# Performance work log

Hardware: AMD Instinct MI355X
Metric: run time of the kernel (lower is better)

The kernel has to match this reference:

```python
import jax, jax.numpy as jnp
import numpy as np

B, T, C, H = 4, 2048, 1024, 1024

def setup_inputs() -> dict:
    key = jax.random.key(0)
    ks = jax.random.split(key, 7)
    s = 0.02
    return {
        "x": jax.random.normal(ks[0], (B, T, C), dtype=jnp.float32),
        "k": jax.random.normal(ks[1], (B, T, C), dtype=jnp.float32),
        "q": jax.random.normal(ks[2], (B, T, C), dtype=jnp.float32),
        "v": jax.random.normal(ks[3], (B, T, C), dtype=jnp.float32),
        "Wk": jax.random.normal(ks[4], (C, H), dtype=jnp.float32) * s,
        "Wq": jax.random.normal(ks[5], (C, H), dtype=jnp.float32) * s,
        "Wv": jax.random.normal(ks[6], (C, H), dtype=jnp.float32) * s,
    }

def reference(x, k, q, v, Wk, Wq, Wv):
    Tcur = x.shape[1]
    kp = jnp.einsum('btc,ch->bth', k, Wk)
    qp = jnp.einsum('btc,ch->bth', q, Wq)
    # NOTE: original torch code (faithfully) projects v with the QUERY weights
    vp = jnp.einsum('btc,ch->bth', v, Wq)
    scale = jnp.asarray(H, jnp.float32) ** -0.5
    weights = jnp.einsum('bth,bsh->bts', qp, kp) * scale  # [B,T,T]
    causal = jnp.tril(jnp.ones((Tcur, Tcur), dtype=bool))
    weights = jnp.where(causal, weights, -jnp.inf)
    weights = jax.nn.softmax(weights, axis=-1)
    # dropout p=0.0 -> identity
    out = jnp.einsum('bts,bsh->bth', weights, vp)
    return out
```

## Files before the change

### kernel.cpp

```cpp
#include <hip/hip_runtime.h>
#include <stdint.h>
#include <math.h>

typedef unsigned short u16;
typedef __attribute__((ext_vector_type(8))) short short8;
typedef __attribute__((ext_vector_type(8))) u16 ushort8;
typedef __attribute__((ext_vector_type(4))) u16 u16x4;
typedef __attribute__((ext_vector_type(4))) float floatx4;

__device__ __forceinline__ u16 f2bf(float f) {
  union { float f; unsigned u; } c; c.f = f;
  unsigned u = c.u;
  return (u16)((u + 0x7fffu + ((u >> 16) & 1u)) >> 16);
}
__device__ __forceinline__ float bf2f(u16 h) {
  union { unsigned u; float f; } c; c.u = (unsigned)h << 16;
  return c.f;
}

__device__ __forceinline__ void async16(const u16* g, u16* l) {
  auto* gp = reinterpret_cast<const __attribute__((address_space(1))) uint32_t*>(
      reinterpret_cast<uintptr_t>(g));
  auto* lp = reinterpret_cast<__attribute__((address_space(3))) uint32_t*>(
      reinterpret_cast<uintptr_t>(l));
  __builtin_amdgcn_global_load_lds(gp, lp, 16, 0, 0);
}

#define WAIT_VM4 0xF74
#define WAIT_VM0 0xF70

template <int OUT_BF16>
__global__ __launch_bounds__(256) void gemm_bt(
    const u16* __restrict__ A, const u16* __restrict__ B, void* __restrict__ Cv,
    int K, int lda, int ldb, int ldc,
    long long sA, long long sB, long long sC,
    float scale, int tri_grid, int causal_klimit, int rev_m,
    int vpt, u16* __restrict__ vpC) {
  int bm, bn;
  if (tri_grid) {
    const int bx = blockIdx.x;
    int i = (int)((sqrtf(8.f * bx + 1.f) - 1.f) * 0.5f);
    while ((i + 1) * (i + 2) / 2 <= bx) ++i;
    while (i * (i + 1) / 2 > bx) --i;
    bm = i;
    bn = bx - i * (i + 1) / 2;
  } else {
    bm = rev_m ? ((int)gridDim.x - 1 - (int)blockIdx.x) : (int)blockIdx.x;
    bn = blockIdx.y;
  }
  const int m0 = bm * 128;
  const int n0 = bn * 128;
  A += (size_t)blockIdx.z * sA;
  B += (size_t)blockIdx.z * sB;

  __shared__ u16 As[2][4096];
  __shared__ u16 Bs[2][4096];

  const int tid = threadIdx.x;
  const int lane = tid & 63;
  const int wid = tid >> 6;
  const int wm = (wid & 1) * 64;
  const int wn = (wid >> 1) * 64;
  const int fr = lane & 15;
  const int fq = lane >> 4;

  floatx4 acc[4][4] = {};

  int kt_end = K >> 5;
  if (causal_klimit) {
    int lim = (m0 >> 5) + 4;
    if (lim < kt_end) kt_end = lim;
  }

  const int rowi = tid >> 2;
  const int segi = tid & 3;
  const int sgz = segi ^ ((rowi >> 1) & 3);
  const u16* gA = A + (size_t)(m0 + rowi) * lda + sgz * 8;
  const u16* gB = B + (size_t)(n0 + rowi) * ldb + sgz * 8;

  int offA[4], offB[4];
#pragma unroll
  for (int i = 0; i < 4; ++i) {
    int ra = wm + i * 16 + fr;
    offA[i] = ra * 32 + (fq ^ ((ra >> 1) & 3)) * 8;
    int rb = wn + i * 16 + fr;
    offB[i] = rb * 32 + (fq ^ ((rb >> 1) & 3)) * 8;
  }

  auto issue = [&](int kt) {
    const int k0 = kt << 5;
    const int odd = kt & 1;
    async16(gA + k0, &As[odd][tid * 8]);
    async16(gA + k0 + (size_t)64 * lda, &As[odd][tid * 8 + 2048]);
    async16(gB + k0, &Bs[odd][tid * 8]);
    async16(gB + k0 + (size_t)64 * ldb, &Bs[odd][tid * 8 + 2048]);
  };

  issue(0);
  for (int kt = 0; kt < kt_end; ++kt) {
    if (kt + 1 < kt_end) {
      issue(kt + 1);
      __builtin_amdgcn_s_waitcnt(WAIT_VM4);
    } else {
      __builtin_amdgcn_s_waitcnt(WAIT_VM0);
    }
    asm volatile("s_barrier" ::: "memory");

    const u16* ab = As[kt & 1];
    const u16* bb = Bs[kt & 1];
    short8 av[4], bv[4];
#pragma unroll
    for (int i = 0; i < 4; ++i) av[i] = *(const short8*)(ab + offA[i]);
#pragma unroll
    for (int j = 0; j < 4; ++j) bv[j] = *(const short8*)(bb + offB[j]);

#pragma unroll
    for (int i = 0; i < 4; ++i)
#pragma unroll
      for (int j = 0; j < 4; ++j)
        acc[i][j] = __builtin_amdgcn_mfma_f32_16x16x32_bf16(av[i], bv[j],
                                                            acc[i][j], 0, 0, 0);
    asm volatile("s_barrier" ::: "memory");
  }

  if (vpt && blockIdx.z == 2) {
#pragma unroll
    for (int i = 0; i < 4; ++i) {
      const int m = m0 + wm + i * 16 + fq * 4;
      const int b = m >> 11, t = m & 2047;
#pragma unroll
      for (int j = 0; j < 4; ++j) {
        const int n = n0 + wn + j * 16 + fr;
        u16x4 o;
#pragma unroll
        for (int r = 0; r < 4; ++r) o[r] = f2bf(acc[i][j][r]);
        *(u16x4*)&vpC[(size_t)b * 2097152 + (size_t)n * 2048 + t] = o;
      }
    }
    return;
  }
  if (OUT_BF16) {
    u16* C = (u16*)Cv + (size_t)blockIdx.z * sC;
#pragma unroll
    for (int i = 0; i < 4; ++i) {
      const int m = m0 + wm + i * 16 + fq * 4;
#pragma unroll
      for (int j = 0; j < 4; ++j) {
        const int n = n0 + wn + j * 16 + fr;
#pragma unroll
        for (int r = 0; r < 4; ++r)
          C[(size_t)(m + r) * ldc + n] = f2bf(acc[i][j][r] * scale);
      }
    }
  } else {
    float* C = (float*)Cv + (size_t)blockIdx.z * sC;
#pragma unroll
    for (int i = 0; i < 4; ++i) {
      const int m = m0 + wm + i * 16 + fq * 4;
#pragma unroll
      for (int j = 0; j < 4; ++j) {
        const int n = n0 + wn + j * 16 + fr;
#pragma unroll
        for (int r = 0; r < 4; ++r)
          C[(size_t)(m + r) * ldc + n] = acc[i][j][r] * scale;
      }
    }
  }
}

__global__ __launch_bounds__(256) void cast3(
    const float* __restrict__ q, const float* __restrict__ k,
    const float* __restrict__ v, u16* __restrict__ out, int n8) {
  int i = blockIdx.x * 256 + threadIdx.x;
  if (i >= n8) return;
  const float* src = blockIdx.y == 0 ? q : (blockIdx.y == 1 ? k : v);
  u16* dst = out + (size_t)blockIdx.y * n8 * 8;
  floatx4 a = ((const floatx4*)src)[i * 2];
  floatx4 b = ((const floatx4*)src)[i * 2 + 1];
  ushort8 o;
#pragma unroll
  for (int j = 0; j < 4; ++j) { o[j] = f2bf(a[j]); o[4 + j] = f2bf(b[j]); }
  ((ushort8*)dst)[i] = o;
}

__global__ __launch_bounds__(256) void transpose_castW(
    const float* __restrict__ Wq, const float* __restrict__ Wk,
    u16* __restrict__ out, int R, int C) {
  __shared__ u16 tile[64][72];
  const float* in = (blockIdx.z == 1) ? Wk : Wq;
  u16* dst = out + (size_t)blockIdx.z * R * C;
  const int r0 = blockIdx.x * 64;
  const int c0 = blockIdx.y * 64;
  const int tid = threadIdx.x;
#pragma unroll
  for (int rnd = 0; rnd < 2; ++rnd) {
    int e = rnd * 256 + tid;
    int rr = e >> 3, seg = e & 7;
    const float* p = &in[(size_t)(r0 + rr) * C + c0 + seg * 8];
    floatx4 a = *(const floatx4*)p;
    floatx4 b = *(const floatx4*)(p + 4);
    u16* tp = &tile[rr][seg * 8];
#pragma unroll
    for (int j = 0; j < 4; ++j) { tp[j] = f2bf(a[j]); tp[4 + j] = f2bf(b[j]); }
  }
  __syncthreads();
#pragma unroll
  for (int rnd = 0; rnd < 2; ++rnd) {
    int e = rnd * 256 + tid;
    int cc = e >> 3, rseg = e & 7;
    ushort8 tv;
#pragma unroll
    for (int j = 0; j < 8; ++j) tv[j] = tile[rseg * 8 + j][cc];
    *(ushort8*)&dst[(size_t)(c0 + cc) * R + r0 + rseg * 8] = tv;
  }
}

__global__ __launch_bounds__(256) void softmax_causal(u16* __restrict__ S,
                                                      int T) {
  const int row = blockIdx.x;
  const int t = row & (T - 1);
  const int len = t + 1;
  u16* srow = S + (size_t)row * T;
  const int tid = threadIdx.x;
  const int base = tid * 8;

  const ushort8 raw = *(const ushort8*)(srow + base);
  float v[8];
  float mx = -1e30f;
#pragma unroll
  for (int j = 0; j < 8; ++j) {
    const float f = bf2f(raw[j]);
    v[j] = (base + j < len) ? f : -1e30f;
    mx = fmaxf(mx, v[j]);
  }
#pragma unroll
  for (int o = 32; o > 0; o >>= 1) mx = fmaxf(mx, __shfl_xor(mx, o, 64));

  __shared__ float red[8];
  if ((tid & 63) == 0) red[tid >> 6] = mx;
  __syncthreads();
  mx = fmaxf(fmaxf(red[0], red[1]), fmaxf(red[2], red[3]));

  float sum = 0.f;
#pragma unroll
  for (int j = 0; j < 8; ++j) {
    const float e = __expf(v[j] - mx);
    v[j] = e;
    sum += e;
  }
#pragma unroll
  for (int o = 32; o > 0; o >>= 1) sum += __shfl_xor(sum, o, 64);
  if ((tid & 63) == 0) red[4 + (tid >> 6)] = sum;
  __syncthreads();
  sum = red[4] + red[5] + red[6] + red[7];
  const float inv = 1.f / sum;

  ushort8 o8;
#pragma unroll
  for (int j = 0; j < 8; ++j) o8[j] = f2bf(v[j] * inv);
  *(ushort8*)(srow + base) = o8;
}

extern "C" void kernel_launch(void* const* d_in, const int* in_sizes, int n_in,
                              void* d_out, int out_size, void* d_ws,
                              size_t ws_size, hipStream_t stream) {
  (void)in_sizes; (void)n_in; (void)out_size; (void)ws_size;
  const float* k  = (const float*)d_in[1];
  const float* q  = (const float*)d_in[2];
  const float* v  = (const float*)d_in[3];
  const float* Wk = (const float*)d_in[4];
  const float* Wq = (const float*)d_in[5];
  float* out = (float*)d_out;

  const int B = 4, T = 2048, C = 1024, H = 1024;
  const int M = B * T;
  const size_t MC = (size_t)M * C, CH = (size_t)C * H, MH = (size_t)M * H;

  u16* qkv  = (u16*)d_ws;
  u16* WT   = qkv + 3 * MC;
  u16* qkvp = WT + 3 * CH;
  u16* vpT  = qkvp + 2 * MH;
  u16* Sb   = vpT + MH;

  const int n8 = (int)(MC / 8);
  cast3<<<dim3(n8 / 256, 3), 256, 0, stream>>>(q, k, v, qkv, n8);
  transpose_castW<<<dim3(C / 64, H / 64, 3), 256, 0, stream>>>(Wq, Wk, WT, C, H);

  gemm_bt<1><<<dim3(M / 128, H / 128, 3), 256, 0, stream>>>(
      qkv, WT, qkvp, C, C, C, H,
      (long long)MC, (long long)CH, (long long)MH, 1.f, 0, 0, 0, 1, vpT);

  gemm_bt<1><<<dim3(136, 1, B), 256, 0, stream>>>(
      qkvp, qkvp + MH, Sb, H, H, H, T,
      (long long)T * H, (long long)T * H, (long long)T * T,
      0.03125f, 1, 0, 0, 0, nullptr);

  softmax_causal<<<dim3(B * T), 256, 0, stream>>>(Sb, T);

  gemm_bt<0><<<dim3(T / 128, H / 128, B), 256, 0, stream>>>(
      Sb, vpT, out, T, T, T, H,
      (long long)T * T, (long long)H * T, (long long)T * H,
      1.f, 0, 1, 1, 0, nullptr);
}
```

Baseline: 318.5 us.

## Split-K the heaviest causal PV row tiles with atomics and reorder triangular grid

The PV GEMM grid grows from 16 to 24 row-blocks per batch: the eight heaviest causal row tiles (rows 8-15) are split along K into two halves, and each half accumulates into a pre-zeroed output with atomic adds. A new zero_splitk kernel clears the bottom half of each batch's output. The triangular QK^T grid is permuted so that short and long tiles are interleaved. The batched projection launch is split into three separate launches so only the V projection writes the transposed layout. The aim is to balance load across CUs for the causal workload, at the cost of extra launches, atomic traffic and a zeroing pass.

Measured after the change: 329.0 us. +3.3%, slower.

```diff
diff --git a/kernel.cpp b/kernel.cpp
--- a/kernel.cpp
+++ b/kernel.cpp
@@ -34,18 +34,32 @@
     const u16* __restrict__ A, const u16* __restrict__ B, void* __restrict__ Cv,
     int K, int lda, int ldb, int ldc,
     long long sA, long long sB, long long sC,
-    float scale, int tri_grid, int causal_klimit, int rev_m,
+    float scale, int tri_grid, int causal_klimit, int splitk,
     int vpt, u16* __restrict__ vpC) {
   int bm, bn;
+  int kt0 = 0;
+  bool part0_heavy = false;
+  bool atomic_out = false;
   if (tri_grid) {
-    const int bx = blockIdx.x;
+    int bx = blockIdx.x;
+    bx = (bx & 7) * 17 + (bx >> 3);
     int i = (int)((sqrtf(8.f * bx + 1.f) - 1.f) * 0.5f);
     while ((i + 1) * (i + 2) / 2 <= bx) ++i;
     while (i * (i + 1) / 2 > bx) --i;
     bm = i;
     bn = bx - i * (i + 1) / 2;
+  } else if (splitk) {
+    const int bx = blockIdx.x;
+    if (bx < 8) {
+      bm = 8 + bx; part0_heavy = true; atomic_out = true;
+    } else if (bx < 16) {
+      bm = 15 - (bx - 8); kt0 = 32; atomic_out = true;
+    } else {
+      bm = 23 - bx;
+    }
+    bn = blockIdx.y;
   } else {
-    bm = rev_m ? ((int)gridDim.x - 1 - (int)blockIdx.x) : (int)blockIdx.x;
+    bm = blockIdx.x;
     bn = blockIdx.y;
   }
   const int m0 = bm * 128;
@@ -71,6 +85,7 @@
     int lim = (m0 >> 5) + 4;
     if (lim < kt_end) kt_end = lim;
   }
+  if (part0_heavy && kt_end > 32) kt_end = 32;
 
   const int rowi = tid >> 2;
   const int segi = tid & 3;
@@ -96,8 +111,8 @@
     async16(gB + k0 + (size_t)64 * ldb, &Bs[odd][tid * 8 + 2048]);
   };
 
-  issue(0);
-  for (int kt = 0; kt < kt_end; ++kt) {
+  issue(kt0);
+  for (int kt = kt0; kt < kt_end; ++kt) {
     if (kt + 1 < kt_end) {
       issue(kt + 1);
       __builtin_amdgcn_s_waitcnt(WAIT_VM4);
@@ -123,7 +138,7 @@
     asm volatile("s_barrier" ::: "memory");
   }
 
-  if (vpt && blockIdx.z == 2) {
+  if (vpt) {
 #pragma unroll
     for (int i = 0; i < 4; ++i) {
       const int m = m0 + wm + i * 16 + fq * 4;
@@ -154,18 +169,41 @@
     }
   } else {
     float* C = (float*)Cv + (size_t)blockIdx.z * sC;
-#pragma unroll
-    for (int i = 0; i < 4; ++i) {
-      const int m = m0 + wm + i * 16 + fq * 4;
-#pragma unroll
-      for (int j = 0; j < 4; ++j) {
-        const int n = n0 + wn + j * 16 + fr;
-#pragma unroll
-        for (int r = 0; r < 4; ++r)
-          C[(size_t)(m + r) * ldc + n] = acc[i][j][r] * scale;
+    if (atomic_out) {
+#pragma unroll
+      for (int i = 0; i < 4; ++i) {
+        const int m = m0 + wm + i * 16 + fq * 4;
+#pragma unroll
+        for (int j = 0; j < 4; ++j) {
+          const int n = n0 + wn + j * 16 + fr;
+#pragma unroll
+          for (int r = 0; r < 4; ++r)
+            unsafeAtomicAdd(&C[(size_t)(m + r) * ldc + n],
+                            acc[i][j][r] * scale);
+        }
       }
-    }
-  }
+    } else {
+#pragma unroll
+      for (int i = 0; i < 4; ++i) {
+        const int m = m0 + wm + i * 16 + fq * 4;
+#pragma unroll
+        for (int j = 0; j < 4; ++j) {
+          const int n = n0 + wn + j * 16 + fr;
+#pragma unroll
+          for (int r = 0; r < 4; ++r)
+            C[(size_t)(m + r) * ldc + n] = acc[i][j][r] * scale;
+        }
+      }
+    }
+  }
+}
+
+__global__ __launch_bounds__(256) void zero_splitk(float* __restrict__ out) {
+  const size_t i = (size_t)blockIdx.x * 256 + threadIdx.x;
+  const size_t z = i >> 18;
+  const size_t r = i & 262143;
+  floatx4* p = (floatx4*)(out + z * 2097152 + 1048576) + r;
+  *p = floatx4{0.f, 0.f, 0.f, 0.f};
 }
 
 __global__ __launch_bounds__(256) void cast3(
@@ -282,13 +320,20 @@
   u16* vpT  = qkvp + 2 * MH;
   u16* Sb   = vpT + MH;
 
+  zero_splitk<<<dim3(4096), 256, 0, stream>>>(out);
+
   const int n8 = (int)(MC / 8);
   cast3<<<dim3(n8 / 256, 3), 256, 0, stream>>>(q, k, v, qkv, n8);
   transpose_castW<<<dim3(C / 64, H / 64, 3), 256, 0, stream>>>(Wq, Wk, WT, C, H);
 
-  gemm_bt<1><<<dim3(M / 128, H / 128, 3), 256, 0, stream>>>(
-      qkv, WT, qkvp, C, C, C, H,
-      (long long)MC, (long long)CH, (long long)MH, 1.f, 0, 0, 0, 1, vpT);
+  gemm_bt<1><<<dim3(M / 128, H / 128, 1), 256, 0, stream>>>(
+      qkv, WT, qkvp, C, C, C, H, 0, 0, 0, 1.f, 0, 0, 0, 0, nullptr);
+  gemm_bt<1><<<dim3(M / 128, H / 128, 1), 256, 0, stream>>>(
+      qkv + MC, WT + CH, qkvp + MH, C, C, C, H, 0, 0, 0, 1.f, 0, 0, 0, 0,
+      nullptr);
+  gemm_bt<1><<<dim3(M / 128, H / 128, 1), 256, 0, stream>>>(
+      qkv + 2 * MC, WT + 2 * CH, qkvp, C, C, C, H, 0, 0, 0, 1.f, 0, 0, 0, 1,
+      vpT);
 
   gemm_bt<1><<<dim3(136, 1, B), 256, 0, stream>>>(
       qkvp, qkvp + MH, Sb, H, H, H, T,
@@ -297,7 +342,7 @@
 
   softmax_causal<<<dim3(B * T), 256, 0, stream>>>(Sb, T);
 
-  gemm_bt<0><<<dim3(T / 128, H / 128, B), 256, 0, stream>>>(
+  gemm_bt<0><<<dim3(24, H / 128, B), 256, 0, stream>>>(
       Sb, vpT, out, T, T, T, H,
       (long long)T * T, (long long)H * T, (long long)T * H,
       1.f, 0, 1, 1, 0, nullptr);
```
